# Optimization experiments

Measured on AMD Instinct MI355X. Metric: run time of the kernel, lower is better.

## Reference

```python
import jax, jax.numpy as jnp
import numpy as np

ROPE_THETA = 10000.0

def apply_rope(x, pos):
    # x: [..., h, s, d], pos: [s] int positions
    d = x.shape[-1]
    inv_freq = ROPE_THETA ** (-jnp.arange(0, d, 2, dtype=jnp.float32) / d)  # [d/2]
    ang = pos.astype(jnp.float32)[:, None] * inv_freq[None, :]              # [s, d/2]
    cos, sin = jnp.cos(ang), jnp.sin(ang)
    x1, x2 = x[..., 0::2], x[..., 1::2]
    r1 = x1 * cos - x2 * sin
    r2 = x1 * sin + x2 * cos
    return jnp.stack([r1, r2], axis=-1).reshape(x.shape)

def setup_inputs() -> dict:
    key = jax.random.key(0)
    ks = jax.random.split(key, 5)
    B, S, D = 2, 2048, 1024
    scale = 1.0 / np.sqrt(D)
    return {
        "x": jax.random.normal(ks[0], (B, S, D), dtype=jnp.float32),
        "token_position": jnp.arange(S, dtype=jnp.int32),
        "Wq": jax.random.normal(ks[1], (D, D), dtype=jnp.float32) * scale,
        "Wk": jax.random.normal(ks[2], (D, D), dtype=jnp.float32) * scale,
        "Wv": jax.random.normal(ks[3], (D, D), dtype=jnp.float32) * scale,
        "Wo": jax.random.normal(ks[4], (D, D), dtype=jnp.float32) * scale,
    }

def reference(x, token_position, Wq, Wk, Wv, Wo):
    H = 16
    B, S, D = x.shape
    ds = D // H
    def split_heads(t):  # [b,s,(h d)] -> [b,h,s,d]
        return t.reshape(B, S, H, ds).transpose(0, 2, 1, 3)
    Q = split_heads(x @ Wq.T)
    K = split_heads(x @ Wk.T)
    V = split_heads(x @ Wv.T)
    Q = apply_rope(Q, token_position)
    K = apply_rope(K, token_position)
    scores = jnp.einsum('bhqd,bhkd->bhqk', Q, K) / jnp.sqrt(jnp.float32(ds))
    causal = jnp.tril(jnp.ones((S, S), dtype=bool))
    scores = jnp.where(causal, scores, jnp.finfo(scores.dtype).min)
    attn = jax.nn.softmax(scores, axis=-1)
    out = jnp.einsum('bhqk,bhkd->bhqd', attn, V)
    out = out.transpose(0, 2, 1, 3).reshape(B, S, D)
    return out @ Wo.T
```

## Files before the change

### kernel.cpp

```cpp
#include <hip/hip_runtime.h>
#include <math.h>

#define BB 2
#define SS 2048
#define DD 1024
#define HH 16
#define M_TOTAL (BB*SS)

typedef __attribute__((ext_vector_type(8))) short bf16x8;
typedef __attribute__((ext_vector_type(4))) float f32x4;

__device__ __forceinline__ short f2bf(float f) {
    union { float f; unsigned u; } v; v.f = f;
    unsigned r = v.u + 0x7fffu + ((v.u >> 16) & 1u);
    return (short)(r >> 16);
}
__device__ __forceinline__ float bf2f(short h) {
    union { unsigned u; float f; } v; v.u = ((unsigned)(unsigned short)h) << 16;
    return v.f;
}
__device__ __forceinline__ unsigned cvt_pk_bf16(float lo, float hi) {
    unsigned r;
    asm volatile("v_cvt_pk_bf16_f32 %0, %1, %2" : "=v"(r) : "v"(lo), "v"(hi));
    return r;
}
__device__ __forceinline__ void gload16(const void* g, void* l) {
    __builtin_amdgcn_global_load_lds(
        (const __attribute__((address_space(1))) unsigned int*)g,
        (__attribute__((address_space(3))) unsigned int*)l, 16, 0, 0);
}

__global__ __launch_bounds__(256) void cvt_all(const float* __restrict__ x,
                                               const float* __restrict__ wq,
                                               const float* __restrict__ wk,
                                               const float* __restrict__ wv,
                                               const float* __restrict__ wo,
                                               short* __restrict__ xb,
                                               short* __restrict__ wqb,
                                               short* __restrict__ wkb,
                                               short* __restrict__ wvb,
                                               short* __restrict__ wob,
                                               float qscale)
{
    const size_t T = (size_t)M_TOTAL * DD;
    const size_t W = (size_t)DD * DD;
    size_t i = ((size_t)blockIdx.x * 256 + threadIdx.x) * 4;
    const float* src; short* dst; float sc = 1.0f; size_t off;
    if (i < T)              { src = x;  dst = xb;  off = i; }
    else if (i < T + W)     { src = wq; dst = wqb; off = i - T; sc = qscale; }
    else if (i < T + 2*W)   { src = wk; dst = wkb; off = i - T - W; }
    else if (i < T + 3*W)   { src = wv; dst = wvb; off = i - T - 2*W; }
    else                    { src = wo; dst = wob; off = i - T - 3*W; }
    float4 v = *(const float4*)(src + off);
    short4 o;
    o.x = f2bf(v.x * sc); o.y = f2bf(v.y * sc);
    o.z = f2bf(v.z * sc); o.w = f2bf(v.w * sc);
    *(short4*)(dst + off) = o;
}

template<int BN, int OUT_BF16>
__global__ __launch_bounds__(256) void gemm_nt_mfma(const short* __restrict__ A,
                                                    const short* __restrict__ W0,
                                                    const short* __restrict__ W1,
                                                    const short* __restrict__ W2,
                                                    void* __restrict__ C0,
                                                    void* __restrict__ C1,
                                                    void* __restrict__ C2,
                                                    int M, int N, int K)
{
    constexpr int WC = BN / 64;
    constexpr int WR = 4 / WC;
    constexpr int MW = 128 / WR;
    constexpr int MT = MW / 16;

    __shared__ __align__(16) short As[128 * 64];
    __shared__ __align__(16) short Bs[BN * 64];

    const short* W = (blockIdx.z == 0) ? W0 : (blockIdx.z == 1) ? W1 : W2;
    void* Cout     = (blockIdx.z == 0) ? C0 : (blockIdx.z == 1) ? C1 : C2;

    const int tid = threadIdx.x;
    const int lane = tid & 63;
    const int w = tid >> 6;
    const int lg = lane >> 4, lc = lane & 15;
    const int wr = w / WC, wc = w % WC;
    const int m0 = blockIdx.x * 128, n0 = blockIdx.y * BN;
    const int wbase = (tid & 0xC0) * 8;

    f32x4 acc[MT][4] = {};

    for (int k0 = 0; k0 < K; k0 += 64) {
        __syncthreads();
#pragma unroll
        for (int it = 0; it < 4; ++it) {
            int cl = it * 256 + tid;
            int r = cl >> 3;
            int c = (cl & 7) ^ (r & 7);
            gload16(A + (size_t)(m0 + r) * K + k0 + c * 8, &As[it * 2048 + wbase]);
        }
#pragma unroll
        for (int it = 0; it < BN / 32; ++it) {
            int cl = it * 256 + tid;
            int r = cl >> 3;
            int c = (cl & 7) ^ (r & 7);
            gload16(W + (size_t)(n0 + r) * K + k0 + c * 8, &Bs[it * 2048 + wbase]);
        }
        __syncthreads();
#pragma unroll
        for (int ks = 0; ks < 2; ++ks) {
            bf16x8 af[MT], bfr[4];
#pragma unroll
            for (int mt = 0; mt < MT; ++mt) {
                int row = wr * MW + mt * 16 + lc;
                af[mt] = *(const bf16x8*)&As[row * 64 + (((ks * 4 + lg) ^ (row & 7)) * 8)];
            }
#pragma unroll
            for (int nt = 0; nt < 4; ++nt) {
                int row = wc * 64 + nt * 16 + lc;
                bfr[nt] = *(const bf16x8*)&Bs[row * 64 + (((ks * 4 + lg) ^ (row & 7)) * 8)];
            }
#pragma unroll
            for (int mt = 0; mt < MT; ++mt)
#pragma unroll
                for (int nt = 0; nt < 4; ++nt)
                    acc[mt][nt] = __builtin_amdgcn_mfma_f32_16x16x32_bf16(
                        af[mt], bfr[nt], acc[mt][nt], 0, 0, 0);
        }
    }
#pragma unroll
    for (int mt = 0; mt < MT; ++mt)
#pragma unroll
        for (int nt = 0; nt < 4; ++nt)
#pragma unroll
            for (int rg = 0; rg < 4; ++rg) {
                int row = m0 + wr * MW + mt * 16 + lg * 4 + rg;
                int col = n0 + wc * 64 + nt * 16 + lc;
                if (OUT_BF16)
                    ((short*)Cout)[(size_t)row * N + col] = f2bf(acc[mt][nt][rg]);
                else
                    ((float*)Cout)[(size_t)row * N + col] = acc[mt][nt][rg];
            }
}

__global__ __launch_bounds__(256) void rope_bf16(short* __restrict__ Q,
                                                 short* __restrict__ K,
                                                 const int* __restrict__ pos)
{
    const int t = blockIdx.x * 256 + threadIdx.x;
    const int ig = t & 7;
    const int h = (t >> 3) & 15;
    const int s = (t >> 7) & 2047;
    const int b = t >> 18;
    const float p = (float)pos[s];
    const size_t off = ((size_t)(b * SS + s)) * DD + h * 64 + ig * 8;
    bf16x8 q8 = *(bf16x8*)(Q + off);
    bf16x8 k8 = *(bf16x8*)(K + off);
#pragma unroll
    for (int j = 0; j < 4; ++j) {
        int i = ig * 4 + j;
        float ang = p * __expf(-(float)i * (9.210340371976184f / 32.0f));
        float c = cosf(ang), sn = sinf(ang);
        float q1 = bf2f(q8[2 * j]), q2 = bf2f(q8[2 * j + 1]);
        q8[2 * j]     = f2bf(q1 * c - q2 * sn);
        q8[2 * j + 1] = f2bf(q1 * sn + q2 * c);
        float k1 = bf2f(k8[2 * j]), k2 = bf2f(k8[2 * j + 1]);
        k8[2 * j]     = f2bf(k1 * c - k2 * sn);
        k8[2 * j + 1] = f2bf(k1 * sn + k2 * c);
    }
    *(bf16x8*)(Q + off) = q8;
    *(bf16x8*)(K + off) = k8;
}

__global__ __launch_bounds__(256) void attn_mfma(const short* __restrict__ Q,
                                                 const short* __restrict__ K,
                                                 const short* __restrict__ V,
                                                 short* __restrict__ O)
{
    __shared__ __align__(16) short Ks[2][64 * 64];
    __shared__ __align__(16) unsigned Vt32[2][64 * 36];
    __shared__ __align__(16) unsigned Pl32[4][16 * 36];

    const int tid = threadIdx.x;
    const int lane = tid & 63;
    const int w = tid >> 6;
    const int lg = lane >> 4, lc = lane & 15;

    const int bid = blockIdx.x;
    const int bh = bid & 31;
    const int pi = bid >> 5;
    const int b = bh >> 4, h = bh & 15;

    const short* Qh = Q + (size_t)b * SS * DD + h * 64;
    const short* Kh = K + (size_t)b * SS * DD + h * 64;
    const short* Vh = V + (size_t)b * SS * DD + h * 64;
    short* Oh = O + (size_t)b * SS * DD + h * 64;

    const int vc = tid & 7, vrp = tid >> 3;
    unsigned* Pw = &Pl32[w][0];
    const int kbase_lds = (tid & 0xC0) * 8;

#pragma unroll 1
    for (int pass = 0; pass < 2; ++pass) {
        const int qt = pass == 0 ? 31 - pi : pi;
        const int qg = qt * 64 + w * 16 + lc;
        bf16x8 qa[2];
#pragma unroll
        for (int ks = 0; ks < 2; ++ks)
            qa[ks] = *(const bf16x8*)(Qh + (size_t)qg * DD + ks * 32 + lg * 8);

        f32x4 oaccT[4] = {};
        float l = 0.0f;

        {
            bf16x8 v0 = *(const bf16x8*)(Vh + (size_t)(2 * vrp) * DD + vc * 8);
            bf16x8 v1 = *(const bf16x8*)(Vh + (size_t)(2 * vrp + 1) * DD + vc * 8);
#pragma unroll
            for (int it = 0; it < 2; ++it) {
                int cl = it * 256 + tid;
                int r = cl >> 3;
                int c = (cl & 7) ^ (r & 7);
                gload16(Kh + (size_t)r * DD + c * 8, &Ks[0][it * 2048 + kbase_lds]);
            }
#pragma unroll
            for (int j = 0; j < 8; ++j) {
                int ds = vc * 8 + j;
                unsigned pk = (unsigned)(unsigned short)v0[j] |
                              ((unsigned)(unsigned short)v1[j] << 16);
                Vt32[0][ds * 36 + (vrp ^ (vc << 2))] = pk;
            }
        }
        __syncthreads();
        int cur = 0;

        for (int kt = 0; kt <= qt; ++kt) {
            bf16x8 v0n, v1n;
            const bool more = (kt < qt);
            if (more) {
                const int nv0 = (kt + 1) * 64;
                v0n = *(const bf16x8*)(Vh + (size_t)(nv0 + 2 * vrp) * DD + vc * 8);
                v1n = *(const bf16x8*)(Vh + (size_t)(nv0 + 2 * vrp + 1) * DD + vc * 8);
#pragma unroll
                for (int it = 0; it < 2; ++it) {
                    int cl = it * 256 + tid;
                    int r = cl >> 3;
                    int c = (cl & 7) ^ (r & 7);
                    gload16(Kh + (size_t)(nv0 + r) * DD + c * 8,
                            &Ks[cur ^ 1][it * 2048 + kbase_lds]);
                }
            }

            f32x4 s[4] = {};
            __builtin_amdgcn_s_setprio(1);
#pragma unroll
            for (int ks = 0; ks < 2; ++ks) {
                int c2 = ks * 4 + lg;
#pragma unroll
                for (int t = 0; t < 4; ++t) {
                    int kr = t * 16 + lc;
                    bf16x8 kb = *(const bf16x8*)&Ks[cur][kr * 64 + ((c2 ^ (kr & 7)) * 8)];
                    s[t] = __builtin_amdgcn_mfma_f32_16x16x32_bf16(kb, qa[ks], s[t], 0, 0, 0);
                }
            }
            __builtin_amdgcn_s_setprio(0);

            if (kt == qt) {
                const int kv0 = kt * 64;
#pragma unroll
                for (int t = 0; t < 4; ++t)
#pragma unroll
                    for (int rg = 0; rg < 4; ++rg)
                        if (kv0 + t * 16 + lg * 4 + rg > qg) s[t][rg] = -1e30f;
            }

#pragma unroll
            for (int t = 0; t < 4; ++t) {
                float p0 = exp2f(s[t][0]);
                float p1 = exp2f(s[t][1]);
                float p2 = exp2f(s[t][2]);
                float p3 = exp2f(s[t][3]);
                l += (p0 + p1) + (p2 + p3);
                Pw[lc * 36 + 8 * t + 2 * lg]     = cvt_pk_bf16(p0, p1);
                Pw[lc * 36 + 8 * t + 2 * lg + 1] = cvt_pk_bf16(p2, p3);
            }

            __builtin_amdgcn_s_setprio(1);
#pragma unroll
            for (int ks = 0; ks < 2; ++ks) {
                bf16x8 pb = *(const bf16x8*)&Pw[lc * 36 + 16 * ks + 4 * lg];
#pragma unroll
                for (int dt = 0; dt < 4; ++dt) {
                    int vr = dt * 16 + lc;
                    bf16x8 vb = *(const bf16x8*)&Vt32[cur][vr * 36 +
                                    4 * ((ks * 4 + lg) ^ ((vr >> 3) & 7))];
                    oaccT[dt] = __builtin_amdgcn_mfma_f32_16x16x32_bf16(vb, pb, oaccT[dt], 0, 0, 0);
                }
            }
            __builtin_amdgcn_s_setprio(0);

            if (more) {
#pragma unroll
                for (int j = 0; j < 8; ++j) {
                    int ds = vc * 8 + j;
                    unsigned pk = (unsigned)(unsigned short)v0n[j] |
                                  ((unsigned)(unsigned short)v1n[j] << 16);
                    Vt32[cur ^ 1][ds * 36 + (vrp ^ (vc << 2))] = pk;
                }
            }
            __syncthreads();
            cur ^= 1;
        }

        l += __shfl_xor(l, 16);
        l += __shfl_xor(l, 32);
        const float inv = 1.0f / l;
#pragma unroll
        for (int dt = 0; dt < 4; ++dt)
#pragma unroll
            for (int rg = 0; rg < 4; ++rg)
                Oh[(size_t)qg * DD + dt * 16 + lg * 4 + rg] = f2bf(oaccT[dt][rg] * inv);
        __syncthreads();
    }
}

extern "C" void kernel_launch(void* const* d_in, const int* in_sizes, int n_in,
                              void* d_out, int out_size, void* d_ws, size_t ws_size,
                              hipStream_t stream)
{
    const float* x   = (const float*)d_in[0];
    const int*   pos = (const int*)d_in[1];
    const float* Wq  = (const float*)d_in[2];
    const float* Wk  = (const float*)d_in[3];
    const float* Wv  = (const float*)d_in[4];
    const float* Wo  = (const float*)d_in[5];
    float* out = (float*)d_out;

    const size_t T = (size_t)M_TOTAL * DD;
    const size_t WSZ = (size_t)DD * DD;
    short* xb  = (short*)d_ws;
    short* wqb = xb + T;
    short* wkb = wqb + WSZ;
    short* wvb = wkb + WSZ;
    short* wob = wvb + WSZ;
    short* Qb  = wob + WSZ;
    short* Kb  = Qb + T;
    short* Vb  = Kb + T;
    short* AOb = Vb + T;

    const int cvt_blocks = (int)((T + 4 * WSZ) / 1024);
    cvt_all<<<cvt_blocks, 256, 0, stream>>>(x, Wq, Wk, Wv, Wo,
                                            xb, wqb, wkb, wvb, wob,
                                            0.18033688011112042f);

    dim3 gqkv(M_TOTAL / 128, DD / 128, 3);
    gemm_nt_mfma<128, 1><<<gqkv, 256, 0, stream>>>(
        xb, wqb, wkb, wvb, Qb, Kb, Vb, M_TOTAL, DD, DD);

    rope_bf16<<<(BB * SS * HH * 8) / 256, 256, 0, stream>>>(Qb, Kb, pos);

    attn_mfma<<<BB * HH * (SS / 128), 256, 0, stream>>>(Qb, Kb, Vb, AOb);

    dim3 go(M_TOTAL / 128, DD / 64, 1);
    gemm_nt_mfma<64, 0><<<go, 256, 0, stream>>>(
        AOb, wob, wob, wob, (void*)out, (void*)out, (void*)out, M_TOTAL, DD, DD);
}
```

Baseline: 116.0 us.

## Widen attention blocks to 128 queries with 8 waves sharing K/V tiles

The attention kernel now uses 512 threads and 8 waves per block, covering 128 query rows per tile instead of 64, and launches half as many blocks. Each staged 64-key K/V tile is shared by twice as many waves, which halves the global K/V traffic and staging work per query. The first four waves skip the final key tile, which lies entirely above their diagonal. V is transposed with 16-bit LDS stores so each thread loads a single row. The cost is a larger block with fewer blocks in flight, idle waves on the skipped tile, and more shared memory.

```diff
diff --git a/kernel.cpp b/kernel.cpp
--- a/kernel.cpp
+++ b/kernel.cpp
@@ -171,14 +171,14 @@
     *(bf16x8*)(K + off) = k8;
 }
 
-__global__ __launch_bounds__(256) void attn_mfma(const short* __restrict__ Q,
+__global__ __launch_bounds__(512) void attn_mfma(const short* __restrict__ Q,
                                                  const short* __restrict__ K,
                                                  const short* __restrict__ V,
                                                  short* __restrict__ O)
 {
     __shared__ __align__(16) short Ks[2][64 * 64];
     __shared__ __align__(16) unsigned Vt32[2][64 * 36];
-    __shared__ __align__(16) unsigned Pl32[4][16 * 36];
+    __shared__ __align__(16) unsigned Pl32[8][16 * 36];
 
     const int tid = threadIdx.x;
     const int lane = tid & 63;
@@ -195,14 +195,19 @@
     const short* Vh = V + (size_t)b * SS * DD + h * 64;
     short* Oh = O + (size_t)b * SS * DD + h * 64;
 
-    const int vc = tid & 7, vrp = tid >> 3;
+    const int kr = tid >> 3;
+    const int kc = (tid & 7) ^ (kr & 7);
+    const int kbase_lds = (tid & 0x1C0) * 8;
+    const int vkey = tid >> 3;
+    const int vc = tid & 7;
+    const int vdw = (vkey >> 1) ^ (vc << 2);
+    const int vhalf = vkey & 1;
     unsigned* Pw = &Pl32[w][0];
-    const int kbase_lds = (tid & 0xC0) * 8;
 
 #pragma unroll 1
     for (int pass = 0; pass < 2; ++pass) {
-        const int qt = pass == 0 ? 31 - pi : pi;
-        const int qg = qt * 64 + w * 16 + lc;
+        const int qt = pass == 0 ? 15 - pi : pi;
+        const int qg = qt * 128 + w * 16 + lc;
         bf16x8 qa[2];
 #pragma unroll
         for (int ks = 0; ks < 2; ++ks)
@@ -211,99 +216,89 @@
         f32x4 oaccT[4] = {};
         float l = 0.0f;
 
+        const int nkt = 2 * qt + 2;
+        const int diag_kt = 2 * qt + (w >> 2);
+        const int skip_kt = (w < 4) ? (2 * qt + 1) : -1;
+
         {
-            bf16x8 v0 = *(const bf16x8*)(Vh + (size_t)(2 * vrp) * DD + vc * 8);
-            bf16x8 v1 = *(const bf16x8*)(Vh + (size_t)(2 * vrp + 1) * DD + vc * 8);
-#pragma unroll
-            for (int it = 0; it < 2; ++it) {
-                int cl = it * 256 + tid;
-                int r = cl >> 3;
-                int c = (cl & 7) ^ (r & 7);
-                gload16(Kh + (size_t)r * DD + c * 8, &Ks[0][it * 2048 + kbase_lds]);
-            }
+            bf16x8 v8 = *(const bf16x8*)(Vh + (size_t)vkey * DD + vc * 8);
+            gload16(Kh + (size_t)kr * DD + kc * 8, &Ks[0][kbase_lds]);
+            short* Vt16 = (short*)&Vt32[0][0];
 #pragma unroll
             for (int j = 0; j < 8; ++j) {
                 int ds = vc * 8 + j;
-                unsigned pk = (unsigned)(unsigned short)v0[j] |
-                              ((unsigned)(unsigned short)v1[j] << 16);
-                Vt32[0][ds * 36 + (vrp ^ (vc << 2))] = pk;
+                Vt16[(ds * 36 + vdw) * 2 + vhalf] = v8[j];
             }
         }
         __syncthreads();
         int cur = 0;
 
-        for (int kt = 0; kt <= qt; ++kt) {
-            bf16x8 v0n, v1n;
-            const bool more = (kt < qt);
+        for (int kt = 0; kt < nkt; ++kt) {
+            bf16x8 v8n;
+            const bool more = (kt + 1 < nkt);
             if (more) {
                 const int nv0 = (kt + 1) * 64;
-                v0n = *(const bf16x8*)(Vh + (size_t)(nv0 + 2 * vrp) * DD + vc * 8);
-                v1n = *(const bf16x8*)(Vh + (size_t)(nv0 + 2 * vrp + 1) * DD + vc * 8);
-#pragma unroll
-                for (int it = 0; it < 2; ++it) {
-                    int cl = it * 256 + tid;
-                    int r = cl >> 3;
-                    int c = (cl & 7) ^ (r & 7);
-                    gload16(Kh + (size_t)(nv0 + r) * DD + c * 8,
-                            &Ks[cur ^ 1][it * 2048 + kbase_lds]);
-                }
-            }
-
-            f32x4 s[4] = {};
-            __builtin_amdgcn_s_setprio(1);
-#pragma unroll
-            for (int ks = 0; ks < 2; ++ks) {
-                int c2 = ks * 4 + lg;
+                v8n = *(const bf16x8*)(Vh + (size_t)(nv0 + vkey) * DD + vc * 8);
+                gload16(Kh + (size_t)(nv0 + kr) * DD + kc * 8,
+                        &Ks[cur ^ 1][kbase_lds]);
+            }
+
+            if (kt != skip_kt) {
+                f32x4 s[4] = {};
+                __builtin_amdgcn_s_setprio(1);
+#pragma unroll
+                for (int ks = 0; ks < 2; ++ks) {
+                    int c2 = ks * 4 + lg;
+#pragma unroll
+                    for (int t = 0; t < 4; ++t) {
+                        int krow = t * 16 + lc;
+                        bf16x8 kb = *(const bf16x8*)&Ks[cur][krow * 64 + ((c2 ^ (krow & 7)) * 8)];
+                        s[t] = __builtin_amdgcn_mfma_f32_16x16x32_bf16(kb, qa[ks], s[t], 0, 0, 0);
+                    }
+                }
+                __builtin_amdgcn_s_setprio(0);
+
+                if (kt == diag_kt) {
+                    const int kv0 = kt * 64;
+#pragma unroll
+                    for (int t = 0; t < 4; ++t)
+#pragma unroll
+                        for (int rg = 0; rg < 4; ++rg)
+                            if (kv0 + t * 16 + lg * 4 + rg > qg) s[t][rg] = -1e30f;
+                }
+
 #pragma unroll
                 for (int t = 0; t < 4; ++t) {
-                    int kr = t * 16 + lc;
-                    bf16x8 kb = *(const bf16x8*)&Ks[cur][kr * 64 + ((c2 ^ (kr & 7)) * 8)];
-                    s[t] = __builtin_amdgcn_mfma_f32_16x16x32_bf16(kb, qa[ks], s[t], 0, 0, 0);
-                }
-            }
-            __builtin_amdgcn_s_setprio(0);
-
-            if (kt == qt) {
-                const int kv0 = kt * 64;
-#pragma unroll
-                for (int t = 0; t < 4; ++t)
-#pragma unroll
-                    for (int rg = 0; rg < 4; ++rg)
-                        if (kv0 + t * 16 + lg * 4 + rg > qg) s[t][rg] = -1e30f;
-            }
-
-#pragma unroll
-            for (int t = 0; t < 4; ++t) {
-                float p0 = exp2f(s[t][0]);
-                float p1 = exp2f(s[t][1]);
-                float p2 = exp2f(s[t][2]);
-                float p3 = exp2f(s[t][3]);
-                l += (p0 + p1) + (p2 + p3);
-                Pw[lc * 36 + 8 * t + 2 * lg]     = cvt_pk_bf16(p0, p1);
-                Pw[lc * 36 + 8 * t + 2 * lg + 1] = cvt_pk_bf16(p2, p3);
-            }
-
-            __builtin_amdgcn_s_setprio(1);
-#pragma unroll
-            for (int ks = 0; ks < 2; ++ks) {
-                bf16x8 pb = *(const bf16x8*)&Pw[lc * 36 + 16 * ks + 4 * lg];
-#pragma unroll
-                for (int dt = 0; dt < 4; ++dt) {
-                    int vr = dt * 16 + lc;
-                    bf16x8 vb = *(const bf16x8*)&Vt32[cur][vr * 36 +
-                                    4 * ((ks * 4 + lg) ^ ((vr >> 3) & 7))];
-                    oaccT[dt] = __builtin_amdgcn_mfma_f32_16x16x32_bf16(vb, pb, oaccT[dt], 0, 0, 0);
-                }
-            }
-            __builtin_amdgcn_s_setprio(0);
+                    float p0 = exp2f(s[t][0]);
+                    float p1 = exp2f(s[t][1]);
+                    float p2 = exp2f(s[t][2]);
+                    float p3 = exp2f(s[t][3]);
+                    l += (p0 + p1) + (p2 + p3);
+                    Pw[lc * 36 + 8 * t + 2 * lg]     = cvt_pk_bf16(p0, p1);
+                    Pw[lc * 36 + 8 * t + 2 * lg + 1] = cvt_pk_bf16(p2, p3);
+                }
+
+                __builtin_amdgcn_s_setprio(1);
+#pragma unroll
+                for (int ks = 0; ks < 2; ++ks) {
+                    bf16x8 pb = *(const bf16x8*)&Pw[lc * 36 + 16 * ks + 4 * lg];
+#pragma unroll
+                    for (int dt = 0; dt < 4; ++dt) {
+                        int vr = dt * 16 + lc;
+                        bf16x8 vb = *(const bf16x8*)&Vt32[cur][vr * 36 +
+                                        4 * ((ks * 4 + lg) ^ ((vr >> 3) & 7))];
+                        oaccT[dt] = __builtin_amdgcn_mfma_f32_16x16x32_bf16(vb, pb, oaccT[dt], 0, 0, 0);
+                    }
+                }
+                __builtin_amdgcn_s_setprio(0);
+            }
 
             if (more) {
+                short* Vt16 = (short*)&Vt32[cur ^ 1][0];
 #pragma unroll
                 for (int j = 0; j < 8; ++j) {
                     int ds = vc * 8 + j;
-                    unsigned pk = (unsigned)(unsigned short)v0n[j] |
-                                  ((unsigned)(unsigned short)v1n[j] << 16);
-                    Vt32[cur ^ 1][ds * 36 + (vrp ^ (vc << 2))] = pk;
+                    Vt16[(ds * 36 + vdw) * 2 + vhalf] = v8n[j];
                 }
             }
             __syncthreads();
@@ -357,7 +352,7 @@
 
     rope_bf16<<<(BB * SS * HH * 8) / 256, 256, 0, stream>>>(Qb, Kb, pos);
 
-    attn_mfma<<<BB * HH * (SS / 128), 256, 0, stream>>>(Qb, Kb, Vb, AOb);
+    attn_mfma<<<BB * HH * (SS / 256), 512, 0, stream>>>(Qb, Kb, Vb, AOb);
 
     dim3 go(M_TOTAL / 128, DD / 64, 1);
     gemm_nt_mfma<64, 0><<<go, 256, 0, stream>>>(
```

Result: slower. 122.2 us (+5.4%).

## Fuse RoPE into QKV GEMM epilogue and attention Q load; one q-tile per block

Applied to the files above, without the earlier changes.

Removes the standalone RoPE kernel. RoPE for K is now applied in the QKV GEMM epilogue (z==1) using a lane shuffle to fetch the pair partner, and RoPE for Q is applied in registers when attention loads Q. Attention blocks now handle one 64-row query tile each instead of two balanced tiles, which doubles the grid but drops the causal load-balancing pairing. This saves a full read and write pass over Q and K plus one launch, at the cost of extra trig work in the epilogues and possible load imbalance across blocks.

```diff
diff --git a/kernel.cpp b/kernel.cpp
--- a/kernel.cpp
+++ b/kernel.cpp
@@ -58,7 +58,7 @@
     *(short4*)(dst + off) = o;
 }
 
-template<int BN, int OUT_BF16>
+template<int BN, int OUT_BF16, int ROPE>
 __global__ __launch_bounds__(256) void gemm_nt_mfma(const short* __restrict__ A,
                                                     const short* __restrict__ W0,
                                                     const short* __restrict__ W1,
@@ -66,6 +66,7 @@
                                                     void* __restrict__ C0,
                                                     void* __restrict__ C1,
                                                     void* __restrict__ C2,
+                                                    const int* __restrict__ pos,
                                                     int M, int N, int K)
 {
     constexpr int WC = BN / 64;
@@ -135,46 +136,30 @@
             for (int rg = 0; rg < 4; ++rg) {
                 int row = m0 + wr * MW + mt * 16 + lg * 4 + rg;
                 int col = n0 + wc * 64 + nt * 16 + lc;
+                float a = acc[mt][nt][rg];
+                if (ROPE) {
+                    if (blockIdx.z == 1) {
+                        float other = __shfl_xor(a, 1);
+                        int s = row & (SS - 1);
+                        int i = (col >> 1) & 31;
+                        float ang = (float)pos[s] *
+                                    __expf(-(float)i * (9.210340371976184f / 32.0f));
+                        float c = cosf(ang), sn = sinf(ang);
+                        a = (lc & 1) ? (other * sn + a * c) : (a * c - other * sn);
+                    }
+                }
                 if (OUT_BF16)
-                    ((short*)Cout)[(size_t)row * N + col] = f2bf(acc[mt][nt][rg]);
+                    ((short*)Cout)[(size_t)row * N + col] = f2bf(a);
                 else
-                    ((float*)Cout)[(size_t)row * N + col] = acc[mt][nt][rg];
-            }
-}
-
-__global__ __launch_bounds__(256) void rope_bf16(short* __restrict__ Q,
-                                                 short* __restrict__ K,
-                                                 const int* __restrict__ pos)
-{
-    const int t = blockIdx.x * 256 + threadIdx.x;
-    const int ig = t & 7;
-    const int h = (t >> 3) & 15;
-    const int s = (t >> 7) & 2047;
-    const int b = t >> 18;
-    const float p = (float)pos[s];
-    const size_t off = ((size_t)(b * SS + s)) * DD + h * 64 + ig * 8;
-    bf16x8 q8 = *(bf16x8*)(Q + off);
-    bf16x8 k8 = *(bf16x8*)(K + off);
-#pragma unroll
-    for (int j = 0; j < 4; ++j) {
-        int i = ig * 4 + j;
-        float ang = p * __expf(-(float)i * (9.210340371976184f / 32.0f));
-        float c = cosf(ang), sn = sinf(ang);
-        float q1 = bf2f(q8[2 * j]), q2 = bf2f(q8[2 * j + 1]);
-        q8[2 * j]     = f2bf(q1 * c - q2 * sn);
-        q8[2 * j + 1] = f2bf(q1 * sn + q2 * c);
-        float k1 = bf2f(k8[2 * j]), k2 = bf2f(k8[2 * j + 1]);
-        k8[2 * j]     = f2bf(k1 * c - k2 * sn);
-        k8[2 * j + 1] = f2bf(k1 * sn + k2 * c);
-    }
-    *(bf16x8*)(Q + off) = q8;
-    *(bf16x8*)(K + off) = k8;
+                    ((float*)Cout)[(size_t)row * N + col] = a;
+            }
 }
 
 __global__ __launch_bounds__(256) void attn_mfma(const short* __restrict__ Q,
                                                  const short* __restrict__ K,
                                                  const short* __restrict__ V,
-                                                 short* __restrict__ O)
+                                                 short* __restrict__ O,
+                                                 const int* __restrict__ pos)
 {
     __shared__ __align__(16) short Ks[2][64 * 64];
     __shared__ __align__(16) unsigned Vt32[2][64 * 36];
@@ -186,8 +171,8 @@
     const int lg = lane >> 4, lc = lane & 15;
 
     const int bid = blockIdx.x;
+    const int qt = 31 - (bid >> 5);
     const int bh = bid & 31;
-    const int pi = bid >> 5;
     const int b = bh >> 4, h = bh & 15;
 
     const short* Qh = Q + (size_t)b * SS * DD + h * 64;
@@ -195,131 +180,138 @@
     const short* Vh = V + (size_t)b * SS * DD + h * 64;
     short* Oh = O + (size_t)b * SS * DD + h * 64;
 
+    const int qg = qt * 64 + w * 16 + lc;
+    const float pq = (float)pos[qg];
+    bf16x8 qa[2];
+#pragma unroll
+    for (int ks = 0; ks < 2; ++ks) {
+        bf16x8 q = *(const bf16x8*)(Qh + (size_t)qg * DD + ks * 32 + lg * 8);
+#pragma unroll
+        for (int j = 0; j < 4; ++j) {
+            int i = ks * 16 + lg * 4 + j;
+            float ang = pq * __expf(-(float)i * (9.210340371976184f / 32.0f));
+            float c = cosf(ang), sn = sinf(ang);
+            float x1 = bf2f(q[2 * j]), x2 = bf2f(q[2 * j + 1]);
+            q[2 * j]     = f2bf(x1 * c - x2 * sn);
+            q[2 * j + 1] = f2bf(x1 * sn + x2 * c);
+        }
+        qa[ks] = q;
+    }
+
+    f32x4 oaccT[4] = {};
+    float l = 0.0f;
+
     const int vc = tid & 7, vrp = tid >> 3;
     unsigned* Pw = &Pl32[w][0];
     const int kbase_lds = (tid & 0xC0) * 8;
 
-#pragma unroll 1
-    for (int pass = 0; pass < 2; ++pass) {
-        const int qt = pass == 0 ? 31 - pi : pi;
-        const int qg = qt * 64 + w * 16 + lc;
-        bf16x8 qa[2];
-#pragma unroll
-        for (int ks = 0; ks < 2; ++ks)
-            qa[ks] = *(const bf16x8*)(Qh + (size_t)qg * DD + ks * 32 + lg * 8);
-
-        f32x4 oaccT[4] = {};
-        float l = 0.0f;
-
-        {
-            bf16x8 v0 = *(const bf16x8*)(Vh + (size_t)(2 * vrp) * DD + vc * 8);
-            bf16x8 v1 = *(const bf16x8*)(Vh + (size_t)(2 * vrp + 1) * DD + vc * 8);
+    {
+        bf16x8 v0 = *(const bf16x8*)(Vh + (size_t)(2 * vrp) * DD + vc * 8);
+        bf16x8 v1 = *(const bf16x8*)(Vh + (size_t)(2 * vrp + 1) * DD + vc * 8);
+#pragma unroll
+        for (int it = 0; it < 2; ++it) {
+            int cl = it * 256 + tid;
+            int r = cl >> 3;
+            int c = (cl & 7) ^ (r & 7);
+            gload16(Kh + (size_t)r * DD + c * 8, &Ks[0][it * 2048 + kbase_lds]);
+        }
+#pragma unroll
+        for (int j = 0; j < 8; ++j) {
+            int ds = vc * 8 + j;
+            unsigned pk = (unsigned)(unsigned short)v0[j] |
+                          ((unsigned)(unsigned short)v1[j] << 16);
+            Vt32[0][ds * 36 + (vrp ^ (vc << 2))] = pk;
+        }
+    }
+    __syncthreads();
+    int cur = 0;
+
+    for (int kt = 0; kt <= qt; ++kt) {
+        bf16x8 v0n, v1n;
+        const bool more = (kt < qt);
+        if (more) {
+            const int nv0 = (kt + 1) * 64;
+            v0n = *(const bf16x8*)(Vh + (size_t)(nv0 + 2 * vrp) * DD + vc * 8);
+            v1n = *(const bf16x8*)(Vh + (size_t)(nv0 + 2 * vrp + 1) * DD + vc * 8);
 #pragma unroll
             for (int it = 0; it < 2; ++it) {
                 int cl = it * 256 + tid;
                 int r = cl >> 3;
                 int c = (cl & 7) ^ (r & 7);
-                gload16(Kh + (size_t)r * DD + c * 8, &Ks[0][it * 2048 + kbase_lds]);
-            }
+                gload16(Kh + (size_t)(nv0 + r) * DD + c * 8,
+                        &Ks[cur ^ 1][it * 2048 + kbase_lds]);
+            }
+        }
+
+        f32x4 s[4] = {};
+        __builtin_amdgcn_s_setprio(1);
+#pragma unroll
+        for (int ks = 0; ks < 2; ++ks) {
+            int c2 = ks * 4 + lg;
+#pragma unroll
+            for (int t = 0; t < 4; ++t) {
+                int kr = t * 16 + lc;
+                bf16x8 kb = *(const bf16x8*)&Ks[cur][kr * 64 + ((c2 ^ (kr & 7)) * 8)];
+                s[t] = __builtin_amdgcn_mfma_f32_16x16x32_bf16(kb, qa[ks], s[t], 0, 0, 0);
+            }
+        }
+        __builtin_amdgcn_s_setprio(0);
+
+        if (kt == qt) {
+            const int kv0 = kt * 64;
+#pragma unroll
+            for (int t = 0; t < 4; ++t)
+#pragma unroll
+                for (int rg = 0; rg < 4; ++rg)
+                    if (kv0 + t * 16 + lg * 4 + rg > qg) s[t][rg] = -1e30f;
+        }
+
+#pragma unroll
+        for (int t = 0; t < 4; ++t) {
+            float p0 = exp2f(s[t][0]);
+            float p1 = exp2f(s[t][1]);
+            float p2 = exp2f(s[t][2]);
+            float p3 = exp2f(s[t][3]);
+            l += (p0 + p1) + (p2 + p3);
+            Pw[lc * 36 + 8 * t + 2 * lg]     = cvt_pk_bf16(p0, p1);
+            Pw[lc * 36 + 8 * t + 2 * lg + 1] = cvt_pk_bf16(p2, p3);
+        }
+
+        __builtin_amdgcn_s_setprio(1);
+#pragma unroll
+        for (int ks = 0; ks < 2; ++ks) {
+            bf16x8 pb = *(const bf16x8*)&Pw[lc * 36 + 16 * ks + 4 * lg];
+#pragma unroll
+            for (int dt = 0; dt < 4; ++dt) {
+                int vr = dt * 16 + lc;
+                bf16x8 vb = *(const bf16x8*)&Vt32[cur][vr * 36 +
+                                4 * ((ks * 4 + lg) ^ ((vr >> 3) & 7))];
+                oaccT[dt] = __builtin_amdgcn_mfma_f32_16x16x32_bf16(vb, pb, oaccT[dt], 0, 0, 0);
+            }
+        }
+        __builtin_amdgcn_s_setprio(0);
+
+        if (more) {
 #pragma unroll
             for (int j = 0; j < 8; ++j) {
                 int ds = vc * 8 + j;
-                unsigned pk = (unsigned)(unsigned short)v0[j] |
-                              ((unsigned)(unsigned short)v1[j] << 16);
-                Vt32[0][ds * 36 + (vrp ^ (vc << 2))] = pk;
+                unsigned pk = (unsigned)(unsigned short)v0n[j] |
+                              ((unsigned)(unsigned short)v1n[j] << 16);
+                Vt32[cur ^ 1][ds * 36 + (vrp ^ (vc << 2))] = pk;
             }
         }
         __syncthreads();
-        int cur = 0;
-
-        for (int kt = 0; kt <= qt; ++kt) {
-            bf16x8 v0n, v1n;
-            const bool more = (kt < qt);
-            if (more) {
-                const int nv0 = (kt + 1) * 64;
-                v0n = *(const bf16x8*)(Vh + (size_t)(nv0 + 2 * vrp) * DD + vc * 8);
-                v1n = *(const bf16x8*)(Vh + (size_t)(nv0 + 2 * vrp + 1) * DD + vc * 8);
-#pragma unroll
-                for (int it = 0; it < 2; ++it) {
-                    int cl = it * 256 + tid;
-                    int r = cl >> 3;
-                    int c = (cl & 7) ^ (r & 7);
-                    gload16(Kh + (size_t)(nv0 + r) * DD + c * 8,
-                            &Ks[cur ^ 1][it * 2048 + kbase_lds]);
-                }
-            }
-
-            f32x4 s[4] = {};
-            __builtin_amdgcn_s_setprio(1);
-#pragma unroll
-            for (int ks = 0; ks < 2; ++ks) {
-                int c2 = ks * 4 + lg;
-#pragma unroll
-                for (int t = 0; t < 4; ++t) {
-                    int kr = t * 16 + lc;
-                    bf16x8 kb = *(const bf16x8*)&Ks[cur][kr * 64 + ((c2 ^ (kr & 7)) * 8)];
-                    s[t] = __builtin_amdgcn_mfma_f32_16x16x32_bf16(kb, qa[ks], s[t], 0, 0, 0);
-                }
-            }
-            __builtin_amdgcn_s_setprio(0);
-
-            if (kt == qt) {
-                const int kv0 = kt * 64;
-#pragma unroll
-                for (int t = 0; t < 4; ++t)
-#pragma unroll
-                    for (int rg = 0; rg < 4; ++rg)
-                        if (kv0 + t * 16 + lg * 4 + rg > qg) s[t][rg] = -1e30f;
-            }
-
-#pragma unroll
-            for (int t = 0; t < 4; ++t) {
-                float p0 = exp2f(s[t][0]);
-                float p1 = exp2f(s[t][1]);
-                float p2 = exp2f(s[t][2]);
-                float p3 = exp2f(s[t][3]);
-                l += (p0 + p1) + (p2 + p3);
-                Pw[lc * 36 + 8 * t + 2 * lg]     = cvt_pk_bf16(p0, p1);
-                Pw[lc * 36 + 8 * t + 2 * lg + 1] = cvt_pk_bf16(p2, p3);
-            }
-
-            __builtin_amdgcn_s_setprio(1);
-#pragma unroll
-            for (int ks = 0; ks < 2; ++ks) {
-                bf16x8 pb = *(const bf16x8*)&Pw[lc * 36 + 16 * ks + 4 * lg];
-#pragma unroll
-                for (int dt = 0; dt < 4; ++dt) {
-                    int vr = dt * 16 + lc;
-                    bf16x8 vb = *(const bf16x8*)&Vt32[cur][vr * 36 +
-                                    4 * ((ks * 4 + lg) ^ ((vr >> 3) & 7))];
-                    oaccT[dt] = __builtin_amdgcn_mfma_f32_16x16x32_bf16(vb, pb, oaccT[dt], 0, 0, 0);
-                }
-            }
-            __builtin_amdgcn_s_setprio(0);
-
-            if (more) {
-#pragma unroll
-                for (int j = 0; j < 8; ++j) {
-                    int ds = vc * 8 + j;
-                    unsigned pk = (unsigned)(unsigned short)v0n[j] |
-                                  ((unsigned)(unsigned short)v1n[j] << 16);
-                    Vt32[cur ^ 1][ds * 36 + (vrp ^ (vc << 2))] = pk;
-                }
-            }
-            __syncthreads();
-            cur ^= 1;
-        }
-
-        l += __shfl_xor(l, 16);
-        l += __shfl_xor(l, 32);
-        const float inv = 1.0f / l;
-#pragma unroll
-        for (int dt = 0; dt < 4; ++dt)
-#pragma unroll
-            for (int rg = 0; rg < 4; ++rg)
-                Oh[(size_t)qg * DD + dt * 16 + lg * 4 + rg] = f2bf(oaccT[dt][rg] * inv);
-        __syncthreads();
+        cur ^= 1;
     }
+
+    l += __shfl_xor(l, 16);
+    l += __shfl_xor(l, 32);
+    const float inv = 1.0f / l;
+#pragma unroll
+    for (int dt = 0; dt < 4; ++dt)
+#pragma unroll
+        for (int rg = 0; rg < 4; ++rg)
+            Oh[(size_t)qg * DD + dt * 16 + lg * 4 + rg] = f2bf(oaccT[dt][rg] * inv);
 }
 
 extern "C" void kernel_launch(void* const* d_in, const int* in_sizes, int n_in,
@@ -352,14 +344,12 @@
                                             0.18033688011112042f);
 
     dim3 gqkv(M_TOTAL / 128, DD / 128, 3);
-    gemm_nt_mfma<128, 1><<<gqkv, 256, 0, stream>>>(
-        xb, wqb, wkb, wvb, Qb, Kb, Vb, M_TOTAL, DD, DD);
-
-    rope_bf16<<<(BB * SS * HH * 8) / 256, 256, 0, stream>>>(Qb, Kb, pos);
-
-    attn_mfma<<<BB * HH * (SS / 128), 256, 0, stream>>>(Qb, Kb, Vb, AOb);
+    gemm_nt_mfma<128, 1, 1><<<gqkv, 256, 0, stream>>>(
+        xb, wqb, wkb, wvb, Qb, Kb, Vb, pos, M_TOTAL, DD, DD);
+
+    attn_mfma<<<BB * HH * (SS / 64), 256, 0, stream>>>(Qb, Kb, Vb, AOb, pos);
 
     dim3 go(M_TOTAL / 128, DD / 64, 1);
-    gemm_nt_mfma<64, 0><<<go, 256, 0, stream>>>(
-        AOb, wob, wob, wob, (void*)out, (void*)out, (void*)out, M_TOTAL, DD, DD);
-}
+    gemm_nt_mfma<64, 0, 0><<<go, 256, 0, stream>>>(
+        AOb, wob, wob, wob, (void*)out, (void*)out, (void*)out, pos, M_TOTAL, DD, DD);
+}
```

Measured after the change: 139.1 us. +20.0%, slower.

## Fuse Q RoPE into attention and launch one query tile per block

Applied to the files above, without the earlier changes.

Applies RoPE to Q inside the attention kernel, right after loading the query fragment, so the separate RoPE pass now only reads and writes K. The attention grid is doubled to one 64-row query tile per block, replacing the two-pass pairing of long and short tiles, and blocks are ordered so the longest tiles start first. The two 32-bit P stores are merged into one 64-bit LDS store. This cuts one Q round trip through global memory and adds parallelism, but gives up the per-block causal load balance the pairing provided and recomputes the sin/cos terms for Q inside attention.

```diff
diff --git a/kernel.cpp b/kernel.cpp
--- a/kernel.cpp
+++ b/kernel.cpp
@@ -142,9 +142,8 @@
             }
 }
 
-__global__ __launch_bounds__(256) void rope_bf16(short* __restrict__ Q,
-                                                 short* __restrict__ K,
-                                                 const int* __restrict__ pos)
+__global__ __launch_bounds__(256) void rope_k(short* __restrict__ K,
+                                              const int* __restrict__ pos)
 {
     const int t = blockIdx.x * 256 + threadIdx.x;
     const int ig = t & 7;
@@ -153,28 +152,24 @@
     const int b = t >> 18;
     const float p = (float)pos[s];
     const size_t off = ((size_t)(b * SS + s)) * DD + h * 64 + ig * 8;
-    bf16x8 q8 = *(bf16x8*)(Q + off);
     bf16x8 k8 = *(bf16x8*)(K + off);
 #pragma unroll
     for (int j = 0; j < 4; ++j) {
         int i = ig * 4 + j;
         float ang = p * __expf(-(float)i * (9.210340371976184f / 32.0f));
         float c = cosf(ang), sn = sinf(ang);
-        float q1 = bf2f(q8[2 * j]), q2 = bf2f(q8[2 * j + 1]);
-        q8[2 * j]     = f2bf(q1 * c - q2 * sn);
-        q8[2 * j + 1] = f2bf(q1 * sn + q2 * c);
         float k1 = bf2f(k8[2 * j]), k2 = bf2f(k8[2 * j + 1]);
         k8[2 * j]     = f2bf(k1 * c - k2 * sn);
         k8[2 * j + 1] = f2bf(k1 * sn + k2 * c);
     }
-    *(bf16x8*)(Q + off) = q8;
     *(bf16x8*)(K + off) = k8;
 }
 
 __global__ __launch_bounds__(256) void attn_mfma(const short* __restrict__ Q,
                                                  const short* __restrict__ K,
                                                  const short* __restrict__ V,
-                                                 short* __restrict__ O)
+                                                 short* __restrict__ O,
+                                                 const int* __restrict__ pos)
 {
     __shared__ __align__(16) short Ks[2][64 * 64];
     __shared__ __align__(16) unsigned Vt32[2][64 * 36];
@@ -186,8 +181,8 @@
     const int lg = lane >> 4, lc = lane & 15;
 
     const int bid = blockIdx.x;
+    const int qt = 31 - (bid >> 5);
     const int bh = bid & 31;
-    const int pi = bid >> 5;
     const int b = bh >> 4, h = bh & 15;
 
     const short* Qh = Q + (size_t)b * SS * DD + h * 64;
@@ -195,131 +190,140 @@
     const short* Vh = V + (size_t)b * SS * DD + h * 64;
     short* Oh = O + (size_t)b * SS * DD + h * 64;
 
+    const int qg = qt * 64 + w * 16 + lc;
+    const float pq = (float)pos[qg];
+    bf16x8 qa[2];
+#pragma unroll
+    for (int ks = 0; ks < 2; ++ks) {
+        bf16x8 q = *(const bf16x8*)(Qh + (size_t)qg * DD + ks * 32 + lg * 8);
+#pragma unroll
+        for (int j = 0; j < 4; ++j) {
+            int i = ks * 16 + lg * 4 + j;
+            float ang = pq * __expf(-(float)i * (9.210340371976184f / 32.0f));
+            float c = cosf(ang), sn = sinf(ang);
+            float x1 = bf2f(q[2 * j]), x2 = bf2f(q[2 * j + 1]);
+            q[2 * j]     = f2bf(x1 * c - x2 * sn);
+            q[2 * j + 1] = f2bf(x1 * sn + x2 * c);
+        }
+        qa[ks] = q;
+    }
+
+    f32x4 oaccT[4] = {};
+    float l = 0.0f;
+
     const int vc = tid & 7, vrp = tid >> 3;
     unsigned* Pw = &Pl32[w][0];
     const int kbase_lds = (tid & 0xC0) * 8;
 
-#pragma unroll 1
-    for (int pass = 0; pass < 2; ++pass) {
-        const int qt = pass == 0 ? 31 - pi : pi;
-        const int qg = qt * 64 + w * 16 + lc;
-        bf16x8 qa[2];
-#pragma unroll
-        for (int ks = 0; ks < 2; ++ks)
-            qa[ks] = *(const bf16x8*)(Qh + (size_t)qg * DD + ks * 32 + lg * 8);
-
-        f32x4 oaccT[4] = {};
-        float l = 0.0f;
-
-        {
-            bf16x8 v0 = *(const bf16x8*)(Vh + (size_t)(2 * vrp) * DD + vc * 8);
-            bf16x8 v1 = *(const bf16x8*)(Vh + (size_t)(2 * vrp + 1) * DD + vc * 8);
+    {
+        bf16x8 v0 = *(const bf16x8*)(Vh + (size_t)(2 * vrp) * DD + vc * 8);
+        bf16x8 v1 = *(const bf16x8*)(Vh + (size_t)(2 * vrp + 1) * DD + vc * 8);
+#pragma unroll
+        for (int it = 0; it < 2; ++it) {
+            int cl = it * 256 + tid;
+            int r = cl >> 3;
+            int c = (cl & 7) ^ (r & 7);
+            gload16(Kh + (size_t)r * DD + c * 8, &Ks[0][it * 2048 + kbase_lds]);
+        }
+#pragma unroll
+        for (int j = 0; j < 8; ++j) {
+            int ds = vc * 8 + j;
+            unsigned pk = (unsigned)(unsigned short)v0[j] |
+                          ((unsigned)(unsigned short)v1[j] << 16);
+            Vt32[0][ds * 36 + (vrp ^ (vc << 2))] = pk;
+        }
+    }
+    __syncthreads();
+    int cur = 0;
+
+    for (int kt = 0; kt <= qt; ++kt) {
+        bf16x8 v0n, v1n;
+        const bool more = (kt < qt);
+        if (more) {
+            const int nv0 = (kt + 1) * 64;
+            v0n = *(const bf16x8*)(Vh + (size_t)(nv0 + 2 * vrp) * DD + vc * 8);
+            v1n = *(const bf16x8*)(Vh + (size_t)(nv0 + 2 * vrp + 1) * DD + vc * 8);
 #pragma unroll
             for (int it = 0; it < 2; ++it) {
                 int cl = it * 256 + tid;
                 int r = cl >> 3;
                 int c = (cl & 7) ^ (r & 7);
-                gload16(Kh + (size_t)r * DD + c * 8, &Ks[0][it * 2048 + kbase_lds]);
-            }
+                gload16(Kh + (size_t)(nv0 + r) * DD + c * 8,
+                        &Ks[cur ^ 1][it * 2048 + kbase_lds]);
+            }
+        }
+
+        f32x4 s[4] = {};
+        __builtin_amdgcn_s_setprio(1);
+#pragma unroll
+        for (int ks = 0; ks < 2; ++ks) {
+            int c2 = ks * 4 + lg;
+#pragma unroll
+            for (int t = 0; t < 4; ++t) {
+                int kr = t * 16 + lc;
+                bf16x8 kb = *(const bf16x8*)&Ks[cur][kr * 64 + ((c2 ^ (kr & 7)) * 8)];
+                s[t] = __builtin_amdgcn_mfma_f32_16x16x32_bf16(kb, qa[ks], s[t], 0, 0, 0);
+            }
+        }
+        __builtin_amdgcn_s_setprio(0);
+
+        if (kt == qt) {
+            const int kv0 = kt * 64;
+#pragma unroll
+            for (int t = 0; t < 4; ++t)
+#pragma unroll
+                for (int rg = 0; rg < 4; ++rg)
+                    if (kv0 + t * 16 + lg * 4 + rg > qg) s[t][rg] = -1e30f;
+        }
+
+#pragma unroll
+        for (int t = 0; t < 4; ++t) {
+            float p0 = exp2f(s[t][0]);
+            float p1 = exp2f(s[t][1]);
+            float p2 = exp2f(s[t][2]);
+            float p3 = exp2f(s[t][3]);
+            l += (p0 + p1) + (p2 + p3);
+            uint2 pk;
+            pk.x = cvt_pk_bf16(p0, p1);
+            pk.y = cvt_pk_bf16(p2, p3);
+            *(uint2*)&Pw[lc * 36 + 8 * t + 2 * lg] = pk;
+        }
+
+        __builtin_amdgcn_s_setprio(1);
+#pragma unroll
+        for (int ks = 0; ks < 2; ++ks) {
+            bf16x8 pb = *(const bf16x8*)&Pw[lc * 36 + 16 * ks + 4 * lg];
+#pragma unroll
+            for (int dt = 0; dt < 4; ++dt) {
+                int vr = dt * 16 + lc;
+                bf16x8 vb = *(const bf16x8*)&Vt32[cur][vr * 36 +
+                                4 * ((ks * 4 + lg) ^ ((vr >> 3) & 7))];
+                oaccT[dt] = __builtin_amdgcn_mfma_f32_16x16x32_bf16(vb, pb, oaccT[dt], 0, 0, 0);
+            }
+        }
+        __builtin_amdgcn_s_setprio(0);
+
+        if (more) {
 #pragma unroll
             for (int j = 0; j < 8; ++j) {
                 int ds = vc * 8 + j;
-                unsigned pk = (unsigned)(unsigned short)v0[j] |
-                              ((unsigned)(unsigned short)v1[j] << 16);
-                Vt32[0][ds * 36 + (vrp ^ (vc << 2))] = pk;
+                unsigned pk = (unsigned)(unsigned short)v0n[j] |
+                              ((unsigned)(unsigned short)v1n[j] << 16);
+                Vt32[cur ^ 1][ds * 36 + (vrp ^ (vc << 2))] = pk;
             }
         }
         __syncthreads();
-        int cur = 0;
-
-        for (int kt = 0; kt <= qt; ++kt) {
-            bf16x8 v0n, v1n;
-            const bool more = (kt < qt);
-            if (more) {
-                const int nv0 = (kt + 1) * 64;
-                v0n = *(const bf16x8*)(Vh + (size_t)(nv0 + 2 * vrp) * DD + vc * 8);
-                v1n = *(const bf16x8*)(Vh + (size_t)(nv0 + 2 * vrp + 1) * DD + vc * 8);
-#pragma unroll
-                for (int it = 0; it < 2; ++it) {
-                    int cl = it * 256 + tid;
-                    int r = cl >> 3;
-                    int c = (cl & 7) ^ (r & 7);
-                    gload16(Kh + (size_t)(nv0 + r) * DD + c * 8,
-                            &Ks[cur ^ 1][it * 2048 + kbase_lds]);
-                }
-            }
-
-            f32x4 s[4] = {};
-            __builtin_amdgcn_s_setprio(1);
-#pragma unroll
-            for (int ks = 0; ks < 2; ++ks) {
-                int c2 = ks * 4 + lg;
-#pragma unroll
-                for (int t = 0; t < 4; ++t) {
-                    int kr = t * 16 + lc;
-                    bf16x8 kb = *(const bf16x8*)&Ks[cur][kr * 64 + ((c2 ^ (kr & 7)) * 8)];
-                    s[t] = __builtin_amdgcn_mfma_f32_16x16x32_bf16(kb, qa[ks], s[t], 0, 0, 0);
-                }
-            }
-            __builtin_amdgcn_s_setprio(0);
-
-            if (kt == qt) {
-                const int kv0 = kt * 64;
-#pragma unroll
-                for (int t = 0; t < 4; ++t)
-#pragma unroll
-                    for (int rg = 0; rg < 4; ++rg)
-                        if (kv0 + t * 16 + lg * 4 + rg > qg) s[t][rg] = -1e30f;
-            }
-
-#pragma unroll
-            for (int t = 0; t < 4; ++t) {
-                float p0 = exp2f(s[t][0]);
-                float p1 = exp2f(s[t][1]);
-                float p2 = exp2f(s[t][2]);
-                float p3 = exp2f(s[t][3]);
-                l += (p0 + p1) + (p2 + p3);
-                Pw[lc * 36 + 8 * t + 2 * lg]     = cvt_pk_bf16(p0, p1);
-                Pw[lc * 36 + 8 * t + 2 * lg + 1] = cvt_pk_bf16(p2, p3);
-            }
-
-            __builtin_amdgcn_s_setprio(1);
-#pragma unroll
-            for (int ks = 0; ks < 2; ++ks) {
-                bf16x8 pb = *(const bf16x8*)&Pw[lc * 36 + 16 * ks + 4 * lg];
-#pragma unroll
-                for (int dt = 0; dt < 4; ++dt) {
-                    int vr = dt * 16 + lc;
-                    bf16x8 vb = *(const bf16x8*)&Vt32[cur][vr * 36 +
-                                    4 * ((ks * 4 + lg) ^ ((vr >> 3) & 7))];
-                    oaccT[dt] = __builtin_amdgcn_mfma_f32_16x16x32_bf16(vb, pb, oaccT[dt], 0, 0, 0);
-                }
-            }
-            __builtin_amdgcn_s_setprio(0);
-
-            if (more) {
-#pragma unroll
-                for (int j = 0; j < 8; ++j) {
-                    int ds = vc * 8 + j;
-                    unsigned pk = (unsigned)(unsigned short)v0n[j] |
-                                  ((unsigned)(unsigned short)v1n[j] << 16);
-                    Vt32[cur ^ 1][ds * 36 + (vrp ^ (vc << 2))] = pk;
-                }
-            }
-            __syncthreads();
-            cur ^= 1;
-        }
-
-        l += __shfl_xor(l, 16);
-        l += __shfl_xor(l, 32);
-        const float inv = 1.0f / l;
-#pragma unroll
-        for (int dt = 0; dt < 4; ++dt)
-#pragma unroll
-            for (int rg = 0; rg < 4; ++rg)
-                Oh[(size_t)qg * DD + dt * 16 + lg * 4 + rg] = f2bf(oaccT[dt][rg] * inv);
-        __syncthreads();
-    }
+        cur ^= 1;
+    }
+
+    l += __shfl_xor(l, 16);
+    l += __shfl_xor(l, 32);
+    const float inv = 1.0f / l;
+#pragma unroll
+    for (int dt = 0; dt < 4; ++dt)
+#pragma unroll
+        for (int rg = 0; rg < 4; ++rg)
+            Oh[(size_t)qg * DD + dt * 16 + lg * 4 + rg] = f2bf(oaccT[dt][rg] * inv);
 }
 
 extern "C" void kernel_launch(void* const* d_in, const int* in_sizes, int n_in,
@@ -355,9 +359,9 @@
     gemm_nt_mfma<128, 1><<<gqkv, 256, 0, stream>>>(
         xb, wqb, wkb, wvb, Qb, Kb, Vb, M_TOTAL, DD, DD);
 
-    rope_bf16<<<(BB * SS * HH * 8) / 256, 256, 0, stream>>>(Qb, Kb, pos);
-
-    attn_mfma<<<BB * HH * (SS / 128), 256, 0, stream>>>(Qb, Kb, Vb, AOb);
+    rope_k<<<(BB * SS * HH * 8) / 256, 256, 0, stream>>>(Kb, pos);
+
+    attn_mfma<<<BB * HH * (SS / 64), 256, 0, stream>>>(Qb, Kb, Vb, AOb, pos);
 
     dim3 go(M_TOTAL / 128, DD / 64, 1);
     gemm_nt_mfma<64, 0><<<go, 256, 0, stream>>>(
```

Measured after the change: 114.3 us. No clear change (-1.4%).
